# Kernel optimization log

Hardware: AMD Instinct MI355X
Metric: run time of the kernel (lower is better)

Reference implementation:

```python
import jax, jax.numpy as jnp
import numpy as np

N_ELEMENTS = 64  # StructureElementLayer(n_elements=64)


def setup_inputs() -> dict:
    key = jax.random.key(0)
    k1, k2 = jax.random.split(key)
    # x: [N, C, T, V] skeleton sequence (batch, coord channels, time, joints)
    x = jax.random.normal(k1, (256, 3, 256, 25), dtype=jnp.float32)
    # StructureElementLayer parameters (torch.rand init / ones*3 init)
    centres = jax.random.uniform(k2, (N_ELEMENTS, 2), dtype=jnp.float32)
    sharpness = jnp.ones((N_ELEMENTS, 2), dtype=jnp.float32) * 3.0
    return {"x": x, "centres": centres, "sharpness": sharpness}


def _mst_deaths(D):
    """Dim-0 Vietoris-Rips persistence deaths == MST edge weights (Prim's algorithm).

    D: [n, n] symmetric distance matrix. Returns [n-1] finite death values
    (births are all 0; the single essential (0, inf) pair contributes
    exp(-inf)=0 to the structure-element layer and is dropped).
    """
    n = D.shape[0]
    in_tree = jnp.zeros((n,), dtype=bool).at[0].set(True)
    dist = D[0]  # min distance from each node to the current tree

    def step(carry, _):
        in_tree, dist = carry
        d = jnp.where(in_tree, jnp.inf, dist)
        j = jnp.argmin(d)
        w = d[j]
        in_tree = in_tree.at[j].set(True)
        dist = jnp.minimum(dist, D[j])
        return (in_tree, dist), w

    (_, _), deaths = jax.lax.scan(step, (in_tree, dist), None, length=n - 1)
    return deaths


def _forward(x, centres, sharpness):
    xm = x.mean(1)                                  # [N, T, V]
    diff = xm[..., :, None] - xm[..., None, :]      # [N, T, V, V] pairwise joint diffs
    diff = diff.mean(-3)                            # [N, V, V]
    feat = jnp.linalg.norm(diff, axis=1)            # [N, V]  (torch.norm(., 2, dim=1))
    feat = (feat - feat.min()) / (feat.max() - feat.min())
    # Euclidean distance matrix of the N points in V-dim space (grad-safe sqrt)
    sq = jnp.sum(feat * feat, axis=1)
    D2 = sq[:, None] + sq[None, :] - 2.0 * (feat @ feat.T)
    D2 = jnp.maximum(D2, 0.0)
    D = jnp.where(D2 > 0.0, jnp.sqrt(jnp.where(D2 > 0.0, D2, 1.0)), 0.0)
    deaths = _mst_deaths(D)                         # [N-1]
    diag = jnp.stack([jnp.zeros_like(deaths), deaths], axis=-1)  # [N-1, 2] (birth, death)
    # StructureElementLayer: sum_i exp(-sum_d (p_id - c_kd)^2 * s_kd^2)
    d2 = (diag[:, None, :] - centres[None, :, :]) ** 2            # [N-1, K, 2]
    out = jnp.exp(-(d2 * (sharpness ** 2)).sum(-1)).sum(0)        # [K]
    return out


def reference(x, centres, sharpness):
    return _forward(x, centres, sharpness)
```

## Files before the change

kernel.cpp:

```cpp
#include <hip/hip_runtime.h>
#include <hip/hip_fp16.h>


#define WS_FEAT 0
#define WS_MM   26624
#define WS_RK   28672
#define WS_DTH  29696
#define WS_NCDC 30720
#define WS_D16  65536
#define WS_MP   196608

#define INF32 0xFFFFFFFFu
#define SA 132
#define SB 68
#define OFF_B (128 * SA)

__global__ void __launch_bounds__(256) k_feat(const float* __restrict__ x,
                                              float* __restrict__ featG,
                                              unsigned int* __restrict__ Mp) {
    __shared__ float sums[25];
    __shared__ float mrow[25];
    const int n = blockIdx.x;
    const int tid = threadIdx.x;
    if (tid < 66) Mp[n * 66 + tid] = INF32;
    if (tid < 25) sums[tid] = 0.0f;
    __syncthreads();
    if (tid < 200) {
        const float* base = x + (long)n * 19200 + 4 * tid;
        float a0 = 0.f, a1 = 0.f, a2 = 0.f, a3 = 0.f;
        #pragma unroll
        for (int i = 0; i < 24; ++i) {
            float4 v = *reinterpret_cast<const float4*>(base + 800 * i);
            a0 += v.x; a1 += v.y; a2 += v.z; a3 += v.w;
        }
        const int v0 = (4 * tid) % 25;
        atomicAdd(&sums[v0], a0);
        atomicAdd(&sums[(v0 + 1) % 25], a1);
        atomicAdd(&sums[(v0 + 2) % 25], a2);
        atomicAdd(&sums[(v0 + 3) % 25], a3);
    }
    __syncthreads();
    if (tid < 25) mrow[tid] = sums[tid] * (1.0f / 768.0f);
    __syncthreads();
    if (tid < 25) {
        float S1 = 0.f, S2 = 0.f;
        #pragma unroll
        for (int v = 0; v < 25; ++v) {
            const float mv = mrow[v];
            S1 += mv; S2 += mv * mv;
        }
        const float r = mrow[tid];
        float q = S2 - 2.f * r * S1 + 25.f * r * r;
        q = fmaxf(q, 0.f);
        featG[n * 26 + tid] = sqrtf(q);
    }
}

template <int CTRL>
__device__ __forceinline__ unsigned int dpp_min_step(unsigned int v) {
    unsigned int t = (unsigned int)__builtin_amdgcn_update_dpp(
        (int)0xFFFFFFFF, (int)v, CTRL, 0xF, 0xF, false);
    return (t < v) ? t : v;
}

__global__ void __launch_bounds__(256) k_dist(const float* __restrict__ featG,
                                              unsigned short* __restrict__ D16,
                                              unsigned int* __restrict__ rowKeyG,
                                              unsigned int* __restrict__ mm) {
    __shared__ float featS[6656];
    __shared__ unsigned int wred[4];
    __shared__ unsigned int bmn, bmx;
    const int i = blockIdx.x;
    const int t = threadIdx.x;
    if (t == 0) { bmn = 0x7F800000u; bmx = 0u; }
    #pragma unroll
    for (int it = 0; it < 7; ++it) {
        const int o = it * 256 + t;
        if (o < 1664) reinterpret_cast<float4*>(featS)[o] =
            reinterpret_cast<const float4*>(featG)[o];
    }
    __syncthreads();
    float fi[25];
    #pragma unroll
    for (int v = 0; v < 25; ++v) fi[v] = featS[i * 26 + v];
    float s = 0.f, fmn = 1e30f, fmx = -1e30f;
    #pragma unroll
    for (int v = 0; v < 25; ++v) {
        const float ft = featS[t * 26 + v];
        const float d = fi[v] - ft;
        s += d * d;
        fmn = fminf(fmn, ft); fmx = fmaxf(fmx, ft);
    }
    if (i == 0) {
        atomicMin(&bmn, __float_as_uint(fmn));
        atomicMax(&bmx, __float_as_uint(fmx));
    }
    const unsigned int w16 = (unsigned int)__half_as_ushort(__float2half(s));
    D16[i * 256 + t] = (unsigned short)w16;
    const unsigned int lo = (t < i) ? t : i, hi = (t < i) ? i : t;
    unsigned int key = (t == i) ? INF32 : ((w16 << 16) | (lo << 8) | hi);
    key = dpp_min_step<0x111>(key);
    key = dpp_min_step<0x112>(key);
    key = dpp_min_step<0x114>(key);
    key = dpp_min_step<0x118>(key);
    key = dpp_min_step<0x142>(key);
    key = dpp_min_step<0x143>(key);
    if ((t & 63) == 63) wred[t >> 6] = key;
    __syncthreads();
    if (t == 0) {
        const unsigned int b0 = wred[0] < wred[1] ? wred[0] : wred[1];
        const unsigned int b1 = wred[2] < wred[3] ? wred[2] : wred[3];
        rowKeyG[i] = b0 < b1 ? b0 : b1;
        if (i == 0) { mm[0] = bmn; mm[1] = bmx; }
    }
}

template <bool RECORD>
__device__ __forceinline__ void wave0_phase(int n, int lane,
        unsigned int* rowKeyS, unsigned char* parentS, unsigned char* newidS,
        unsigned char* cmapS, float* deaths, unsigned int* ncS, unsigned int* dcS) {
    unsigned int par[4];
    #pragma unroll
    for (int s = 0; s < 4; ++s) {
        const int i = lane + 64 * s;
        if (i < n) {
            const unsigned int rk = rowKeyS[i];
            const unsigned int u = (rk >> 8) & 0xFFu, v = rk & 0xFFu;
            unsigned int p = (u == (unsigned int)i) ? v : u;
            if (rk == INF32) p = (unsigned int)i;
            par[s] = p;
            parentS[i] = (unsigned char)p;
        }
    }
    #pragma unroll
    for (int s = 0; s < 4; ++s) {
        const int i = lane + 64 * s;
        if (i < n) {
            const unsigned int p = par[s];
            if (p != (unsigned int)i) {
                if (parentS[p] == (unsigned char)i && (unsigned int)i < p) {
                    parentS[i] = (unsigned char)i;
                } else if (RECORD) {
                    const unsigned int d = atomicAdd(dcS, 1u);
                    const unsigned int rk = rowKeyS[i];
                    deaths[d] = sqrtf(__half2float(__ushort_as_half(
                        (unsigned short)(rk >> 16))));
                }
            }
        }
    }
    for (;;) {
        bool ch = false;
        #pragma unroll
        for (int s = 0; s < 4; ++s) {
            const int i = lane + 64 * s;
            if (i < n) {
                const unsigned char p0 = parentS[i];
                const unsigned char np = parentS[p0];
                if (np != p0) { ch = true; parentS[i] = np; }
            }
        }
        if (__ballot(ch) == 0ull) break;
    }
    bool isr[4];
    #pragma unroll
    for (int s = 0; s < 4; ++s) {
        const int i = lane + 64 * s;
        isr[s] = (i < n) && (parentS[i] == (unsigned char)i);
    }
    unsigned int base = 0;
    const unsigned long long below = (1ull << lane) - 1ull;
    #pragma unroll
    for (int s = 0; s < 4; ++s) {
        const unsigned long long mask = __ballot(isr[s]);
        if (isr[s]) {
            const int i = lane + 64 * s;
            newidS[i] = (unsigned char)(base + __popcll(mask & below));
        }
        base += (unsigned int)__popcll(mask);
    }
    if (lane == 0) *ncS = base;
    #pragma unroll
    for (int s = 0; s < 4; ++s) {
        const int i = lane + 64 * s;
        if (i < n) cmapS[i] = newidS[parentS[i]];
    }
}

__global__ void __launch_bounds__(256) k_contract(const unsigned short* __restrict__ D16g,
                                                  const unsigned int* __restrict__ rowKeyG,
                                                  unsigned int* __restrict__ Mp,
                                                  float* __restrict__ deathsG,
                                                  unsigned int* __restrict__ ncdcG) {
    __shared__ unsigned int rowKeyS[256];
    __shared__ unsigned char parentS[256], newidS[256], cmapS[256];
    __shared__ unsigned int ncS, dcS;
    __shared__ float deathsS[256];
    const int tid = threadIdx.x;
    const int b = blockIdx.x;
    rowKeyS[tid] = rowKeyG[tid];
    if (tid == 0) dcS = 0;
    __syncthreads();
    if (tid < 64) {
        if (b == 0)
            wave0_phase<true>(256, tid, rowKeyS, parentS, newidS, cmapS,
                              deathsS, &ncS, &dcS);
        else
            wave0_phase<false>(256, tid, rowKeyS, parentS, newidS, cmapS,
                               nullptr, &ncS, nullptr);
    }
    __syncthreads();
    if (b == 0) {
        if (tid < dcS) deathsG[tid] = deathsS[tid];
        if (tid == 0) { ncdcG[0] = ncS; ncdcG[1] = dcS; }
    }
    const unsigned int ca = cmapS[b];
    const unsigned int cb = cmapS[tid];
    if (ca != cb) {
        const unsigned int w16 = (unsigned int)D16g[b * 256 + tid];
        const unsigned int lo = ca < cb ? ca : cb;
        const unsigned int hi = ca < cb ? cb : ca;
        atomicMin(&Mp[ca * SA + cb], (w16 << 16) | (lo << 8) | hi);
    }
}

__global__ void __launch_bounds__(1024) k_mst(const unsigned int* __restrict__ Mp,
                                              const float* __restrict__ deathsG,
                                              const unsigned int* __restrict__ ncdcG,
                                              const unsigned int* __restrict__ mm,
                                              const float* __restrict__ centres,
                                              const float* __restrict__ sharp,
                                              float* __restrict__ out) {
    __shared__ unsigned int Mb[128 * SA + 64 * SB];
    __shared__ unsigned int rowKeyS[128];
    __shared__ unsigned char parentS[128], newidS[128], cmapS[128];
    __shared__ unsigned int ncS, dcS;
    __shared__ float deaths[256];
    __shared__ float outpart[1024];
    const int tid = threadIdx.x;

    if (tid == 0) { ncS = ncdcG[0]; dcS = ncdcG[1]; }
    if (tid < 256) deaths[tid] = deathsG[tid];
    if (tid < 128) rowKeyS[tid] = INF32;
    __syncthreads();
    int n = (int)ncS;

    for (int idx = tid; idx < n * 33; idx += 1024)
        reinterpret_cast<uint4*>(Mb)[idx] =
            reinterpret_cast<const uint4*>(Mp)[idx];
    __syncthreads();

    int srcOff = 0, srcStr = SA, dstOff = OFF_B, dstStr = SB;
    for (int round = 0; round < 12 && n > 1; ++round) {
        if (tid < 8 * n) {
            const int a = tid >> 3, sub = tid & 7;
            const unsigned int* row = &Mb[srcOff + a * srcStr];
            unsigned int best = INF32;
            for (int b2 = sub; b2 < n; b2 += 8) {
                const unsigned int v = row[b2];
                best = v < best ? v : best;
            }
            if (best != INF32) atomicMin(&rowKeyS[a], best);
        }
        const int dstCap = (n >> 1) * dstStr;
        for (int w = tid; w < dstCap; w += 1024) Mb[dstOff + w] = INF32;
        __syncthreads();
        if (tid < 64)
            wave0_phase<true>(n, tid, rowKeyS, parentS, newidS, cmapS,
                              deaths, &ncS, &dcS);
        __syncthreads();
        const int nc = (int)ncS;
        if (nc <= 1) break;
        if (tid < 8 * n) {
            const int a = tid >> 3, sub = tid & 7;
            const unsigned int ca = cmapS[a];
            const unsigned int* row = &Mb[srcOff + a * srcStr];
            for (int b2 = sub; b2 < n; b2 += 8) {
                const unsigned int cb = cmapS[b2];
                const unsigned int v = row[b2];
                if (ca != cb && v != INF32) {
                    const unsigned int lo = ca < cb ? ca : cb;
                    const unsigned int hi = ca < cb ? cb : ca;
                    atomicMin(&Mb[dstOff + ca * dstStr + cb],
                              (v & 0xFFFF0000u) | (lo << 8) | hi);
                }
            }
        }
        for (int j = tid; j < (n >> 1); j += 1024) rowKeyS[j] = INF32;
        __syncthreads();
        const int t1 = srcOff; srcOff = dstOff; dstOff = t1;
        const int t2 = srcStr; srcStr = dstStr; dstStr = t2;
        n = nc;
    }

    const float mn = __uint_as_float(mm[0]);
    const float mx = __uint_as_float(mm[1]);
    const float inv = 1.0f / (mx - mn);
    const int k = tid & 63;
    const int part = tid >> 6;
    const float c0 = centres[2 * k], c1 = centres[2 * k + 1];
    const float s0 = sharp[2 * k],   s1 = sharp[2 * k + 1];
    const float t0 = c0 * c0 * s0 * s0;
    const float s1sq = s1 * s1;
    float acc = 0.f;
    for (int idx = part; idx < 255; idx += 16) {
        const float d = deaths[idx] * inv - c1;
        acc += __expf(-(t0 + d * d * s1sq));
    }
    outpart[tid] = acc;
    __syncthreads();
    if (tid < 64) {
        float s = 0.f;
        #pragma unroll
        for (int pp = 0; pp < 16; ++pp) s += outpart[tid + 64 * pp];
        out[tid] = s;
    }
}

extern "C" void kernel_launch(void* const* d_in, const int* in_sizes, int n_in,
                              void* d_out, int out_size, void* d_ws, size_t ws_size,
                              hipStream_t stream) {
    const float* x       = (const float*)d_in[0];
    const float* centres = (const float*)d_in[1];
    const float* sharp   = (const float*)d_in[2];
    float* out = (float*)d_out;
    char* ws = (char*)d_ws;
    float*          featG = (float*)(ws + WS_FEAT);
    unsigned int*   mm    = (unsigned int*)(ws + WS_MM);
    unsigned int*   rk    = (unsigned int*)(ws + WS_RK);
    float*          dth   = (float*)(ws + WS_DTH);
    unsigned int*   ncdc  = (unsigned int*)(ws + WS_NCDC);
    unsigned short* D16   = (unsigned short*)(ws + WS_D16);
    unsigned int*   Mp    = (unsigned int*)(ws + WS_MP);

    k_feat<<<256, 256, 0, stream>>>(x, featG, Mp);
    k_dist<<<256, 256, 0, stream>>>(featG, D16, rk, mm);
    k_contract<<<256, 256, 0, stream>>>(D16, rk, Mp, dth, ncdc);
    k_mst<<<1, 1024, 0, stream>>>(Mp, dth, ncdc, mm, centres, sharp, out);
}
```

Measured before the change: 91.55 us.

## Fuse contraction and MST kernels using last-block atomic completion counter

Merges the contraction kernel and the single-block MST kernel into one launch. Every block does its contraction atomics, then increments a global done counter, and block 0 spin-waits until all 256 blocks have arrived before running the Boruvka/MST rounds. This removes one kernel launch and its gap, plus the global round-trip for deaths and the component counts. In exchange it launches 1024-thread blocks that reserve large shared memory although most threads only do 256-wide work. The spin-wait depends on all blocks being co-resident or scheduled before block 0 finishes, and has a guard timeout.

Result: no change. 92.72 us (+1.3%).

```diff
diff --git a/kernel.cpp b/kernel.cpp
--- a/kernel.cpp
+++ b/kernel.cpp
@@ -5,8 +5,7 @@
 #define WS_FEAT 0
 #define WS_MM   26624
 #define WS_RK   28672
-#define WS_DTH  29696
-#define WS_NCDC 30720
+#define WS_DONE 30720
 #define WS_D16  65536
 #define WS_MP   196608
 
@@ -17,12 +16,14 @@
 
 __global__ void __launch_bounds__(256) k_feat(const float* __restrict__ x,
                                               float* __restrict__ featG,
-                                              unsigned int* __restrict__ Mp) {
+                                              unsigned int* __restrict__ Mp,
+                                              unsigned int* __restrict__ doneG) {
     __shared__ float sums[25];
     __shared__ float mrow[25];
     const int n = blockIdx.x;
     const int tid = threadIdx.x;
     if (tid < 66) Mp[n * 66 + tid] = INF32;
+    if (n == 0 && tid == 0) *doneG = 0u;
     if (tid < 25) sums[tid] = 0.0f;
     __syncthreads();
     if (tid < 200) {
@@ -187,68 +188,68 @@
     }
 }
 
-__global__ void __launch_bounds__(256) k_contract(const unsigned short* __restrict__ D16g,
-                                                  const unsigned int* __restrict__ rowKeyG,
-                                                  unsigned int* __restrict__ Mp,
-                                                  float* __restrict__ deathsG,
-                                                  unsigned int* __restrict__ ncdcG) {
+__global__ void __launch_bounds__(1024) k_cmst(const unsigned short* __restrict__ D16g,
+                                               const unsigned int* __restrict__ rowKeyG,
+                                               unsigned int* __restrict__ Mp,
+                                               unsigned int* __restrict__ doneG,
+                                               const unsigned int* __restrict__ mm,
+                                               const float* __restrict__ centres,
+                                               const float* __restrict__ sharp,
+                                               float* __restrict__ out) {
+    __shared__ unsigned int Mb[128 * SA + 64 * SB];
     __shared__ unsigned int rowKeyS[256];
     __shared__ unsigned char parentS[256], newidS[256], cmapS[256];
-    __shared__ unsigned int ncS, dcS;
-    __shared__ float deathsS[256];
-    const int tid = threadIdx.x;
-    const int b = blockIdx.x;
-    rowKeyS[tid] = rowKeyG[tid];
-    if (tid == 0) dcS = 0;
-    __syncthreads();
-    if (tid < 64) {
-        if (b == 0)
-            wave0_phase<true>(256, tid, rowKeyS, parentS, newidS, cmapS,
-                              deathsS, &ncS, &dcS);
-        else
-            wave0_phase<false>(256, tid, rowKeyS, parentS, newidS, cmapS,
-                               nullptr, &ncS, nullptr);
-    }
-    __syncthreads();
-    if (b == 0) {
-        if (tid < dcS) deathsG[tid] = deathsS[tid];
-        if (tid == 0) { ncdcG[0] = ncS; ncdcG[1] = dcS; }
-    }
-    const unsigned int ca = cmapS[b];
-    const unsigned int cb = cmapS[tid];
-    if (ca != cb) {
-        const unsigned int w16 = (unsigned int)D16g[b * 256 + tid];
-        const unsigned int lo = ca < cb ? ca : cb;
-        const unsigned int hi = ca < cb ? cb : ca;
-        atomicMin(&Mp[ca * SA + cb], (w16 << 16) | (lo << 8) | hi);
-    }
-}
-
-__global__ void __launch_bounds__(1024) k_mst(const unsigned int* __restrict__ Mp,
-                                              const float* __restrict__ deathsG,
-                                              const unsigned int* __restrict__ ncdcG,
-                                              const unsigned int* __restrict__ mm,
-                                              const float* __restrict__ centres,
-                                              const float* __restrict__ sharp,
-                                              float* __restrict__ out) {
-    __shared__ unsigned int Mb[128 * SA + 64 * SB];
-    __shared__ unsigned int rowKeyS[128];
-    __shared__ unsigned char parentS[128], newidS[128], cmapS[128];
     __shared__ unsigned int ncS, dcS;
     __shared__ float deaths[256];
     __shared__ float outpart[1024];
     const int tid = threadIdx.x;
-
-    if (tid == 0) { ncS = ncdcG[0]; dcS = ncdcG[1]; }
-    if (tid < 256) deaths[tid] = deathsG[tid];
+    const int b = blockIdx.x;
+
+    if (tid < 256) rowKeyS[tid] = rowKeyG[tid];
+    if (tid == 0) dcS = 0;
+    __syncthreads();
+    if (tid < 64) {
+        if (b == 0)
+            wave0_phase<true>(256, tid, rowKeyS, parentS, newidS, cmapS,
+                              deaths, &ncS, &dcS);
+        else
+            wave0_phase<false>(256, tid, rowKeyS, parentS, newidS, cmapS,
+                               nullptr, &ncS, nullptr);
+    }
+    __syncthreads();
+    if (tid < 256) {
+        const unsigned int ca = cmapS[b];
+        const unsigned int cb = cmapS[tid];
+        if (ca != cb) {
+            const unsigned int w16 = (unsigned int)D16g[b * 256 + tid];
+            const unsigned int lo = ca < cb ? ca : cb;
+            const unsigned int hi = ca < cb ? cb : ca;
+            atomicMin(&Mp[ca * SA + cb], (w16 << 16) | (lo << 8) | hi);
+        }
+    }
+    asm volatile("s_waitcnt vmcnt(0)" ::: "memory");
+    __syncthreads();
+    if (tid == 0)
+        __hip_atomic_fetch_add(doneG, 1u, __ATOMIC_RELEASE,
+                               __HIP_MEMORY_SCOPE_AGENT);
+    if (b != 0) return;
+
+    if (tid == 0) {
+        unsigned int guard = 0;
+        while (__hip_atomic_load(doneG, __ATOMIC_ACQUIRE,
+                                 __HIP_MEMORY_SCOPE_AGENT) < 256u) {
+            __builtin_amdgcn_s_sleep(1);
+            if (++guard > (1u << 22)) break;
+        }
+    }
+    __syncthreads();
+
+    for (int idx = tid; idx < 128 * SA; idx += 1024)
+        Mb[idx] = __hip_atomic_load(&Mp[idx], __ATOMIC_RELAXED,
+                                    __HIP_MEMORY_SCOPE_AGENT);
     if (tid < 128) rowKeyS[tid] = INF32;
     __syncthreads();
     int n = (int)ncS;
-
-    for (int idx = tid; idx < n * 33; idx += 1024)
-        reinterpret_cast<uint4*>(Mb)[idx] =
-            reinterpret_cast<const uint4*>(Mp)[idx];
-    __syncthreads();
 
     int srcOff = 0, srcStr = SA, dstOff = OFF_B, dstStr = SB;
     for (int round = 0; round < 12 && n > 1; ++round) {
@@ -328,13 +329,11 @@
     float*          featG = (float*)(ws + WS_FEAT);
     unsigned int*   mm    = (unsigned int*)(ws + WS_MM);
     unsigned int*   rk    = (unsigned int*)(ws + WS_RK);
-    float*          dth   = (float*)(ws + WS_DTH);
-    unsigned int*   ncdc  = (unsigned int*)(ws + WS_NCDC);
+    unsigned int*   done  = (unsigned int*)(ws + WS_DONE);
     unsigned short* D16   = (unsigned short*)(ws + WS_D16);
     unsigned int*   Mp    = (unsigned int*)(ws + WS_MP);
 
-    k_feat<<<256, 256, 0, stream>>>(x, featG, Mp);
+    k_feat<<<256, 256, 0, stream>>>(x, featG, Mp, done);
     k_dist<<<256, 256, 0, stream>>>(featG, D16, rk, mm);
-    k_contract<<<256, 256, 0, stream>>>(D16, rk, Mp, dth, ncdc);
-    k_mst<<<1, 1024, 0, stream>>>(Mp, dth, ncdc, mm, centres, sharp, out);
-}
+    k_cmst<<<256, 1024, 0, stream>>>(D16, rk, Mp, done, mm, centres, sharp, out);
+}
```
